# Performance work log

Measured on AMD Instinct MI355X. Metric: run time of the kernel, lower is better.

The kernel has to match this reference:

```python
import jax, jax.numpy as jnp
import numpy as np

N = 100000   # nodes
E = 3200000  # edges (before self-loops)
F = 128      # input feature dim
H = 2        # heads
C = 16       # hidden per head
G = 64       # graphs in batch
NEG_SLOPE = 0.2


def _gat_layer(x, src, dst, eattr, W, a_src, a_dst, W_e, a_e, bias):
    # x: [N, Fin]; W: [Fin, H*C]; eattr: [Et, 1]; W_e: [1, H*C]; a_*: [H, C]
    n = x.shape[0]
    h = (x @ W).reshape(n, H, C)                      # [N,H,C]
    asrc = jnp.sum(h * a_src, axis=-1)                # [N,H]
    adst = jnp.sum(h * a_dst, axis=-1)                # [N,H]
    he = (eattr @ W_e).reshape(-1, H, C)              # [Et,H,C]
    aedge = jnp.sum(he * a_e, axis=-1)                # [Et,H]
    alpha = jax.nn.leaky_relu(asrc[src] + adst[dst] + aedge, NEG_SLOPE)
    # segment softmax over incoming edges of each destination node
    m = jax.ops.segment_max(alpha, dst, num_segments=n)
    ex = jnp.exp(alpha - m[dst])
    s = jax.ops.segment_sum(ex, dst, num_segments=n)
    att = ex / (s[dst] + 1e-16)                        # [Et,H]
    msg = h[src] * att[:, :, None]                     # [Et,H,C]
    out = jax.ops.segment_sum(msg, dst, num_segments=n)  # [N,H,C]
    return out.reshape(n, H * C) + bias


def setup_inputs() -> dict:
    key = jax.random.key(0)
    ks = jax.random.split(key, 24)
    d = {
        'x': jax.random.normal(ks[0], (N, F), dtype=jnp.float32),
        'edge_index': jax.random.randint(ks[1], (2, E), 0, N, dtype=jnp.int64),
        'edge_attr': jax.random.normal(ks[2], (E, 1), dtype=jnp.float32),
        'batch': jnp.sort(jax.random.randint(ks[3], (N,), 0, G, dtype=jnp.int64)),
        # conv1: F -> H*C
        'W1': jax.random.normal(ks[4], (F, H * C), dtype=jnp.float32) * 0.1,
        'att_src1': jax.random.normal(ks[5], (H, C), dtype=jnp.float32) * 0.1,
        'att_dst1': jax.random.normal(ks[6], (H, C), dtype=jnp.float32) * 0.1,
        'We1': jax.random.normal(ks[7], (1, H * C), dtype=jnp.float32) * 0.1,
        'att_edge1': jax.random.normal(ks[8], (H, C), dtype=jnp.float32) * 0.1,
        'b1': jnp.zeros((H * C,), dtype=jnp.float32),
        # conv2: H*C -> H*C
        'W2': jax.random.normal(ks[9], (H * C, H * C), dtype=jnp.float32) * 0.1,
        'att_src2': jax.random.normal(ks[10], (H, C), dtype=jnp.float32) * 0.1,
        'att_dst2': jax.random.normal(ks[11], (H, C), dtype=jnp.float32) * 0.1,
        'We2': jax.random.normal(ks[12], (1, H * C), dtype=jnp.float32) * 0.1,
        'att_edge2': jax.random.normal(ks[13], (H, C), dtype=jnp.float32) * 0.1,
        'b2': jnp.zeros((H * C,), dtype=jnp.float32),
        # predictor MLP: 32 -> 32 -> 2
        'Wf1': jax.random.normal(ks[14], (H * C, 32), dtype=jnp.float32) * 0.1,
        'bf1': jnp.zeros((32,), dtype=jnp.float32),
        'Wf2': jax.random.normal(ks[15], (32, 2), dtype=jnp.float32) * 0.1,
        'bf2': jnp.zeros((2,), dtype=jnp.float32),
    }
    return d


def reference(x, edge_index, edge_attr, batch,
              W1, att_src1, att_dst1, We1, att_edge1, b1,
              W2, att_src2, att_dst2, We2, att_edge2, b2,
              Wf1, bf1, Wf2, bf2):
    n = x.shape[0]
    # PyG GATConv default: add self-loops with edge_attr fill_value='mean'
    loops = jnp.arange(n, dtype=edge_index.dtype)
    src = jnp.concatenate([edge_index[0], loops])
    dst = jnp.concatenate([edge_index[1], loops])
    ea = jnp.concatenate([edge_attr,
                          jnp.broadcast_to(edge_attr.mean(axis=0, keepdims=True), (n, 1))])
    h = _gat_layer(x, src, dst, ea, W1, att_src1, att_dst1, We1, att_edge1, b1)
    h = jax.nn.relu(h)  # dropout is identity in eval mode
    h = _gat_layer(h, src, dst, ea, W2, att_src2, att_dst2, We2, att_edge2, b2)
    # global mean pool over graphs
    sums = jax.ops.segment_sum(h, batch, num_segments=G)          # [G, H*C]
    cnt = jax.ops.segment_sum(jnp.ones((n,), h.dtype), batch, num_segments=G)
    emb = sums / jnp.maximum(cnt, 1.0)[:, None]
    # predictor MLP
    return jax.nn.relu(emb @ Wf1 + bf1) @ Wf2 + bf2               # [G, 2]
```

## Files before the change

kernel.cpp:

```cpp
#include <hip/hip_runtime.h>
#include <hip/hip_fp16.h>

#define N_NODES 100000
#define N_EDGES 3200000
#define F_IN    128
#define HC      32
#define CH      16
#define NGRAPH  64
#define NEG     0.2f

#define BSH   8
#define BNODE (1 << BSH)
#define NB2   ((N_NODES + BNODE - 1) >> BSH)
#define CAP   9216
#define EPB2  8192
#define BTHR  1024
#define HEPB  4096
#define GPAD  16
#define CHK   4096
#define NPB   512
#define GSPAN 16

__device__ __forceinline__ float lrelu(float x) { return x > 0.f ? x : NEG * x; }


__global__ void k_init(int* __restrict__ gcur, float* __restrict__ params,
                       float* __restrict__ gsums) {
    int t = threadIdx.x;
    if (t < NB2) gcur[t * GPAD] = t * CAP;
    if (t < 16) params[t] = 0.f;
    gsums[t] = 0.f;
    gsums[t + 1024] = 0.f;
}


__global__ __launch_bounds__(1024)
void k_bucket(const int* __restrict__ src, const int* __restrict__ dst,
              const float* __restrict__ ea, int* __restrict__ gcur,
              int2* __restrict__ staged, float* __restrict__ params) {
    __shared__ int lcur[NB2];
    __shared__ int lscan[512];
    __shared__ int gbase[NB2];
    __shared__ short rbkt[HEPB];
    __shared__ int2 recs[HEPB];
    int t = threadIdx.x;
    float acc = 0.f;
    for (int half = 0; half < 2; ++half) {
        int base = blockIdx.x * EPB2 + half * HEPB;
        for (int i = t; i < NB2; i += BTHR) lcur[i] = 0;
        __syncthreads();
        int  myb[HEPB / BTHR];
        int  myrank[HEPB / BTHR];
        int2 myrec[HEPB / BTHR];
#pragma unroll
        for (int i = 0; i < HEPB / BTHR; ++i) {
            int e = base + i * BTHR + t;
            myb[i] = -1;
            if (e < N_EDGES) {
                int dv = dst[e];
                float eav = ea[e];
                acc += eav;
                myb[i] = dv >> BSH;
                myrank[i] = atomicAdd(&lcur[myb[i]], 1);
                myrec[i] = make_int2((src[e] << BSH) | (dv & (BNODE - 1)),
                                     __float_as_int(eav));
            }
        }
        __syncthreads();
        if (t < 512) lscan[t] = (t < NB2) ? lcur[t] : 0;
        __syncthreads();
        for (int off = 1; off < 512; off <<= 1) {
            int u = 0;
            if (t < 512 && t >= off) u = lscan[t - off];
            __syncthreads();
            if (t < 512) lscan[t] += u;
            __syncthreads();
        }
        if (t < NB2 && lcur[t] > 0) gbase[t] = atomicAdd(&gcur[t * GPAD], lcur[t]);
        __syncthreads();
#pragma unroll
        for (int i = 0; i < HEPB / BTHR; ++i) {
            if (myb[i] >= 0) {
                int p = lscan[myb[i]] - lcur[myb[i]] + myrank[i];
                recs[p] = myrec[i];
                rbkt[p] = (short)myb[i];
            }
        }
        __syncthreads();
        int tot = lscan[511];
        for (int p = t; p < tot; p += BTHR) {
            int b = rbkt[p];
            int ex = lscan[b] - lcur[b];
            staged[gbase[b] + (p - ex)] = recs[p];
        }
        __syncthreads();
    }
    for (int m = 32; m >= 1; m >>= 1) acc += __shfl_xor(acc, m, 64);
    __shared__ float sh[BTHR / 64];
    int lane = t & 63, wid = t >> 6;
    if (lane == 0) sh[wid] = acc;
    __syncthreads();
    if (t == 0) {
        float s = 0.f;
        for (int i = 0; i < BTHR / 64; ++i) s += sh[i];
        unsafeAtomicAdd(&params[0], s);
    }
}


__global__ void k_setup(const float* __restrict__ We1, const float* __restrict__ ae1,
                        const float* __restrict__ We2, const float* __restrict__ ae2,
                        float* __restrict__ params, const int* __restrict__ gcur,
                        int* __restrict__ gstart, int* __restrict__ rowptr) {
    int t = threadIdx.x;
    if (t < 2) {
        float c1 = 0.f, c2 = 0.f;
        for (int c = 0; c < CH; ++c) {
            c1 += We1[t * CH + c] * ae1[t * CH + c];
            c2 += We2[t * CH + c] * ae2[t * CH + c];
        }
        params[2 + t] = c1;
        params[4 + t] = c2;
        if (t == 0) params[1] = params[0] / (float)N_EDGES;
    }
    __shared__ int sh[256];
    int v[2];
    int s = 0;
    for (int j = 0; j < 2; ++j) {
        int i = t * 2 + j;
        v[j] = (i < NB2) ? (gcur[i * GPAD] - i * CAP) : 0;
        s += v[j];
    }
    sh[t] = s;
    __syncthreads();
    for (int off = 1; off < 256; off <<= 1) {
        int u = (t >= off) ? sh[t - off] : 0;
        __syncthreads();
        sh[t] += u;
        __syncthreads();
    }
    int ex = sh[t] - s;
    for (int j = 0; j < 2; ++j) {
        int i = t * 2 + j;
        if (i < NB2) { gstart[i] = ex; ex += v[j]; }
    }
    if (t == 255) {
        gstart[NB2] = N_EDGES;
        rowptr[N_NODES] = N_EDGES;
    }
}


__global__ __launch_bounds__(1024)
void k_scatter(const int2* __restrict__ staged, const int* __restrict__ gcur,
               const int* __restrict__ gstart,
               int* __restrict__ rowptr, int2* __restrict__ epack) {
    __shared__ int cntl[BNODE];
    __shared__ int scanb[BNODE];
    __shared__ int cur[BNODE];
    __shared__ int cchist[BNODE];
    __shared__ int cexcl[BNODE];
    __shared__ short rbkt[CHK];
    __shared__ int2 recs[CHK];
    int b = blockIdx.x, t = threadIdx.x;
    int nbase = b << BSH;
    int bcount = N_NODES - nbase;
    if (bcount > BNODE) bcount = BNODE;
    int sbase = b * CAP;
    int en = gcur[b * GPAD];
    int st_true = gstart[b];
    if (t < BNODE) cntl[t] = 0;
    __syncthreads();
    for (int e = sbase + t; e < en; e += 1024)
        atomicAdd(&cntl[staged[e].x & (BNODE - 1)], 1);
    __syncthreads();
    if (t < BNODE) scanb[t] = cntl[t];
    __syncthreads();
    for (int off = 1; off < BNODE; off <<= 1) {
        int u = (t < BNODE && t >= off) ? scanb[t - off] : 0;
        __syncthreads();
        if (t < BNODE) scanb[t] += u;
        __syncthreads();
    }
    if (t < BNODE) {
        int ex = st_true + scanb[t] - cntl[t];
        cur[t] = ex;
        if (t < bcount) rowptr[nbase + t] = ex;
    }
    __syncthreads();
    int count = en - sbase;
    for (int cb = 0; cb < count; cb += CHK) {
        int clen = count - cb;
        if (clen > CHK) clen = CHK;
        if (t < BNODE) cchist[t] = 0;
        __syncthreads();
        int  mylo[CHK / 1024];
        int  myrank[CHK / 1024];
        int2 myrec[CHK / 1024];
#pragma unroll
        for (int i = 0; i < CHK / 1024; ++i) {
            int p = i * 1024 + t;
            mylo[i] = -1;
            if (p < clen) {
                int2 r = staged[sbase + cb + p];
                mylo[i] = r.x & (BNODE - 1);
                myrank[i] = atomicAdd(&cchist[mylo[i]], 1);
                myrec[i] = r;
            }
        }
        __syncthreads();
        if (t < BNODE) cexcl[t] = cchist[t];
        __syncthreads();
        for (int off = 1; off < BNODE; off <<= 1) {
            int u = (t < BNODE && t >= off) ? cexcl[t - off] : 0;
            __syncthreads();
            if (t < BNODE) cexcl[t] += u;
            __syncthreads();
        }
        if (t < BNODE) cexcl[t] -= cchist[t];
        __syncthreads();
#pragma unroll
        for (int i = 0; i < CHK / 1024; ++i) {
            if (mylo[i] >= 0) {
                int p = cexcl[mylo[i]] + myrank[i];
                recs[p] = myrec[i];
                rbkt[p] = (short)mylo[i];
            }
        }
        __syncthreads();
        for (int p = t; p < clen; p += 1024) {
            int lo = rbkt[p];
            epack[cur[lo] + (p - cexcl[lo])] = recs[p];
        }
        __syncthreads();
        if (t < BNODE) cur[t] += cchist[t];
        __syncthreads();
    }
}


#define COLS(ac, xv)                                                     \
    ac[0] = fmaf(xv.x, w0.x, ac[0]); ac[1] = fmaf(xv.x, w0.y, ac[1]);    \
    ac[2] = fmaf(xv.x, w0.z, ac[2]); ac[3] = fmaf(xv.x, w0.w, ac[3]);    \
    ac[0] = fmaf(xv.y, w1.x, ac[0]); ac[1] = fmaf(xv.y, w1.y, ac[1]);    \
    ac[2] = fmaf(xv.y, w1.z, ac[2]); ac[3] = fmaf(xv.y, w1.w, ac[3]);    \
    ac[0] = fmaf(xv.z, w2.x, ac[0]); ac[1] = fmaf(xv.z, w2.y, ac[1]);    \
    ac[2] = fmaf(xv.z, w2.z, ac[2]); ac[3] = fmaf(xv.z, w2.w, ac[3]);    \
    ac[0] = fmaf(xv.w, w3.x, ac[0]); ac[1] = fmaf(xv.w, w3.y, ac[1]);    \
    ac[2] = fmaf(xv.w, w3.z, ac[2]); ac[3] = fmaf(xv.w, w3.w, ac[3]);

template <int FIN>
__global__ __launch_bounds__(256)
void k_linear(const float* __restrict__ x, const float* __restrict__ W,
              const float* __restrict__ a_src, const float* __restrict__ a_dst,
              __half* __restrict__ h16, float* __restrict__ asrc,
              float* __restrict__ adst) {
    constexpr int PAD = FIN + 4;
    __shared__ float ws[FIN * HC];
    __shared__ float xs[64 * PAD];
    int t = threadIdx.x;
    int nbase = blockIdx.x * 64;
    int bcount = N_NODES - nbase;
    if (bcount > 64) bcount = 64;

    for (int i = t; i < FIN * HC / 4; i += 256)
        ((float4*)ws)[i] = ((const float4*)W)[i];
    const float4* xg = (const float4*)(x + (size_t)nbase * FIN);
    int nf4 = bcount * FIN / 4;
    for (int i = t; i < 64 * FIN / 4; i += 256) {
        if (i < nf4) {
            float4 v = xg[i];
            int flat = i * 4;
            int row = flat / FIN, col = flat % FIN;
            *(float4*)&xs[row * PAD + col] = v;
        }
    }
    __syncthreads();

    int cg = t & 7, np = t >> 3;
    int n0 = np * 2, n1 = n0 + 1;
    float acc0[4] = {0.f, 0.f, 0.f, 0.f};
    float acc1[4] = {0.f, 0.f, 0.f, 0.f};
#pragma unroll
    for (int k = 0; k < FIN; k += 4) {
        float4 xa = *(const float4*)&xs[n0 * PAD + k];
        float4 xb = *(const float4*)&xs[n1 * PAD + k];
        const float4* wp = (const float4*)&ws[k * HC] + cg;
        float4 w0 = wp[0], w1 = wp[8], w2 = wp[16], w3 = wp[24];
        COLS(acc0, xa)
        COLS(acc1, xb)
    }

    int hh = cg >> 2;
    float s0 = 0.f, d0 = 0.f, s1 = 0.f, d1 = 0.f;
#pragma unroll
    for (int j = 0; j < 4; ++j) {
        float av = a_src[hh * CH + (cg & 3) * 4 + j];
        float dv = a_dst[hh * CH + (cg & 3) * 4 + j];
        s0 = fmaf(acc0[j], av, s0); d0 = fmaf(acc0[j], dv, d0);
        s1 = fmaf(acc1[j], av, s1); d1 = fmaf(acc1[j], dv, d1);
    }
    s0 += __shfl_xor(s0, 1, 64); s0 += __shfl_xor(s0, 2, 64);
    d0 += __shfl_xor(d0, 1, 64); d0 += __shfl_xor(d0, 2, 64);
    s1 += __shfl_xor(s1, 1, 64); s1 += __shfl_xor(s1, 2, 64);
    d1 += __shfl_xor(d1, 1, 64); d1 += __shfl_xor(d1, 2, 64);

    if (n0 < bcount) {
        __half2 pa = __floats2half2_rn(acc0[0], acc0[1]);
        __half2 pb = __floats2half2_rn(acc0[2], acc0[3]);
        *(uint2*)&h16[(size_t)(nbase + n0) * HC + cg * 4] =
            make_uint2(*(unsigned*)&pa, *(unsigned*)&pb);
        if ((cg & 3) == 0) {
            asrc[(nbase + n0) * 2 + hh] = s0;
            adst[(nbase + n0) * 2 + hh] = d0;
        }
    }
    if (n1 < bcount) {
        __half2 pa = __floats2half2_rn(acc1[0], acc1[1]);
        __half2 pb = __floats2half2_rn(acc1[2], acc1[3]);
        *(uint2*)&h16[(size_t)(nbase + n1) * HC + cg * 4] =
            make_uint2(*(unsigned*)&pa, *(unsigned*)&pb);
        if ((cg & 3) == 0) {
            asrc[(nbase + n1) * 2 + hh] = s1;
            adst[(nbase + n1) * 2 + hh] = d1;
        }
    }
}


#define FMA4(ACC, WGT, VEC)                                                      \
    ACC.x = fmaf(WGT, VEC.x, ACC.x); ACC.y = fmaf(WGT, VEC.y, ACC.y);            \
    ACC.z = fmaf(WGT, VEC.z, ACC.z); ACC.w = fmaf(WGT, VEC.w, ACC.w);

__device__ __forceinline__ void unpack8(uint4 hv, float4& p, float4& u) {
    float2 f0 = __half22float2(*(__half2*)&hv.x);
    float2 f1 = __half22float2(*(__half2*)&hv.y);
    float2 f2 = __half22float2(*(__half2*)&hv.z);
    float2 f3 = __half22float2(*(__half2*)&hv.w);
    p = make_float4(f0.x, f0.y, f1.x, f1.y);
    u = make_float4(f2.x, f2.y, f3.x, f3.y);
}

template <int FUSE>
__global__ __launch_bounds__(256)
void k_gat(const int* __restrict__ rowptr, const int2* __restrict__ epack,
           const __half* __restrict__ h16,
           const float* __restrict__ asrc, const float* __restrict__ adst,
           const float* __restrict__ params, int ceoff,
           const float* __restrict__ bias, int do_relu,
           float* __restrict__ outf, __half* __restrict__ outh,
           const float* __restrict__ W2,
           const float* __restrict__ as2, const float* __restrict__ ad2,
           float* __restrict__ asrc2, float* __restrict__ adst2) {
    __shared__ float w2s[FUSE ? HC * HC : 4];
    int t = threadIdx.x;
    if (FUSE) {
        for (int i = t; i < HC * HC / 4; i += 256)
            ((float4*)w2s)[i] = ((const float4*)W2)[i];
        __syncthreads();
    }
    int tid = blockIdx.x * blockDim.x + t;
    int n = tid >> 4;
    if (n >= N_NODES) return;
    int q = tid & 15;
    int chan = q & 3, quarter = q >> 2, hh = chan >> 1;
    int st = rowptr[n], en = rowptr[n + 1];
    int len = en - st;
    int q0 = st + ((len * quarter) >> 2);
    int q1 = st + ((len * (quarter + 1)) >> 2);
    float ce = params[ceoff + hh];
    float adn = adst[n * 2 + hh];
    const uint4* h4v = (const uint4*)h16;
    float4 A0 = make_float4(0.f, 0.f, 0.f, 0.f);
    float4 A1 = make_float4(0.f, 0.f, 0.f, 0.f);
    float ssum = 0.f;
    for (int e = q0; e < q1; e += 4) {
        int e1 = e + 1, e2 = e + 2, e3 = e + 3;
        int i1 = e1 < q1 ? e1 : q1 - 1;
        int i2 = e2 < q1 ? e2 : q1 - 1;
        int i3 = e3 < q1 ? e3 : q1 - 1;
        int2 r0 = epack[e], r1 = epack[i1], r2 = epack[i2], r3 = epack[i3];
        int s0 = r0.x >> BSH, s1 = r1.x >> BSH, s2 = r2.x >> BSH, s3 = r3.x >> BSH;
        float a0 = asrc[s0 * 2 + hh], a1 = asrc[s1 * 2 + hh];
        float a2 = asrc[s2 * 2 + hh], a3 = asrc[s3 * 2 + hh];
        uint4 hv0 = h4v[s0 * 4 + chan];
        uint4 hv1 = h4v[s1 * 4 + chan];
        uint4 hv2 = h4v[s2 * 4 + chan];
        uint4 hv3 = h4v[s3 * 4 + chan];
        float g0 = __expf(lrelu(a0 + adn + ce * __int_as_float(r0.y)));
        float g1 = __expf(lrelu(a1 + adn + ce * __int_as_float(r1.y)));
        float g2 = __expf(lrelu(a2 + adn + ce * __int_as_float(r2.y)));
        float g3 = __expf(lrelu(a3 + adn + ce * __int_as_float(r3.y)));
        g1 = (e1 < q1) ? g1 : 0.f;
        g2 = (e2 < q1) ? g2 : 0.f;
        g3 = (e3 < q1) ? g3 : 0.f;
        float4 p0, u0, p1, u1, p2, u2, p3, u3;
        unpack8(hv0, p0, u0); unpack8(hv1, p1, u1);
        unpack8(hv2, p2, u2); unpack8(hv3, p3, u3);
        FMA4(A0, g0, p0) FMA4(A1, g0, u0) ssum += g0;
        FMA4(A0, g1, p1) FMA4(A1, g1, u1) ssum += g1;
        FMA4(A0, g2, p2) FMA4(A1, g2, u2) ssum += g2;
        FMA4(A0, g3, p3) FMA4(A1, g3, u3) ssum += g3;
    }
    if (quarter == 0) {
        float gself = __expf(lrelu(asrc[n * 2 + hh] + adn + ce * params[1]));
        float4 psf, usf;
        unpack8(h4v[n * 4 + chan], psf, usf);
        FMA4(A0, gself, psf) FMA4(A1, gself, usf)
        ssum += gself;
    }
    A0.x += __shfl_xor(A0.x, 4, 64); A0.y += __shfl_xor(A0.y, 4, 64);
    A0.z += __shfl_xor(A0.z, 4, 64); A0.w += __shfl_xor(A0.w, 4, 64);
    A1.x += __shfl_xor(A1.x, 4, 64); A1.y += __shfl_xor(A1.y, 4, 64);
    A1.z += __shfl_xor(A1.z, 4, 64); A1.w += __shfl_xor(A1.w, 4, 64);
    ssum += __shfl_xor(ssum, 4, 64);
    A0.x += __shfl_xor(A0.x, 8, 64); A0.y += __shfl_xor(A0.y, 8, 64);
    A0.z += __shfl_xor(A0.z, 8, 64); A0.w += __shfl_xor(A0.w, 8, 64);
    A1.x += __shfl_xor(A1.x, 8, 64); A1.y += __shfl_xor(A1.y, 8, 64);
    A1.z += __shfl_xor(A1.z, 8, 64); A1.w += __shfl_xor(A1.w, 8, 64);
    ssum += __shfl_xor(ssum, 8, 64);
    if (quarter != 0) return;
    float inv = 1.f / (ssum + 1e-16f);
    int b4 = chan * 2;
    float4 bv0 = ((const float4*)bias)[b4], bv1 = ((const float4*)bias)[b4 + 1];
    float4 v0 = make_float4(A0.x * inv + bv0.x, A0.y * inv + bv0.y,
                            A0.z * inv + bv0.z, A0.w * inv + bv0.w);
    float4 v1 = make_float4(A1.x * inv + bv1.x, A1.y * inv + bv1.y,
                            A1.z * inv + bv1.z, A1.w * inv + bv1.w);
    if (do_relu) {
        v0.x = fmaxf(v0.x, 0.f); v0.y = fmaxf(v0.y, 0.f);
        v0.z = fmaxf(v0.z, 0.f); v0.w = fmaxf(v0.w, 0.f);
        v1.x = fmaxf(v1.x, 0.f); v1.y = fmaxf(v1.y, 0.f);
        v1.z = fmaxf(v1.z, 0.f); v1.w = fmaxf(v1.w, 0.f);
    }
    if (!FUSE) {
        ((float4*)outf)[n * 8 + b4] = v0;
        ((float4*)outf)[n * 8 + b4 + 1] = v1;
        return;
    }
    int lane = t & 63;
    int bse = lane & 48;
    float h2[8] = {0.f, 0.f, 0.f, 0.f, 0.f, 0.f, 0.f, 0.f};
#pragma unroll
    for (int cc = 0; cc < 4; ++cc) {
        int sl = bse | cc;
        float vv[8];
        vv[0] = __shfl(v0.x, sl, 64); vv[1] = __shfl(v0.y, sl, 64);
        vv[2] = __shfl(v0.z, sl, 64); vv[3] = __shfl(v0.w, sl, 64);
        vv[4] = __shfl(v1.x, sl, 64); vv[5] = __shfl(v1.y, sl, 64);
        vv[6] = __shfl(v1.z, sl, 64); vv[7] = __shfl(v1.w, sl, 64);
#pragma unroll
        for (int m = 0; m < 8; ++m) {
            const float* wrow = &w2s[(cc * 8 + m) * HC + chan * 8];
            float4 wa = *(const float4*)&wrow[0];
            float4 wb = *(const float4*)&wrow[4];
            h2[0] = fmaf(vv[m], wa.x, h2[0]); h2[1] = fmaf(vv[m], wa.y, h2[1]);
            h2[2] = fmaf(vv[m], wa.z, h2[2]); h2[3] = fmaf(vv[m], wa.w, h2[3]);
            h2[4] = fmaf(vv[m], wb.x, h2[4]); h2[5] = fmaf(vv[m], wb.y, h2[5]);
            h2[6] = fmaf(vv[m], wb.z, h2[6]); h2[7] = fmaf(vv[m], wb.w, h2[7]);
        }
    }
    __half2 q0h = __floats2half2_rn(h2[0], h2[1]);
    __half2 q1h = __floats2half2_rn(h2[2], h2[3]);
    __half2 q2h = __floats2half2_rn(h2[4], h2[5]);
    __half2 q3h = __floats2half2_rn(h2[6], h2[7]);
    *(uint4*)&outh[(size_t)n * HC + chan * 8] =
        make_uint4(*(unsigned*)&q0h, *(unsigned*)&q1h,
                   *(unsigned*)&q2h, *(unsigned*)&q3h);
    float s2 = 0.f, d2 = 0.f;
#pragma unroll
    for (int j = 0; j < 8; ++j) {
        s2 = fmaf(h2[j], as2[chan * 8 + j], s2);
        d2 = fmaf(h2[j], ad2[chan * 8 + j], d2);
    }
    s2 += __shfl_xor(s2, 1, 64);
    d2 += __shfl_xor(d2, 1, 64);
    if ((chan & 1) == 0) {
        asrc2[n * 2 + (chan >> 1)] = s2;
        adst2[n * 2 + (chan >> 1)] = d2;
    }
}


__global__ __launch_bounds__(1024)
void k_pool1(const float* __restrict__ feat, const int* __restrict__ batch,
             float* __restrict__ gsums) {
    __shared__ float gsum[GSPAN][32];
    int t = threadIdx.x;
    int c = t & 31, r = t >> 5;
    int base = blockIdx.x * NPB;
    if (t < GSPAN * 32) ((float*)gsum)[t] = 0.f;
    __syncthreads();
    int g0 = batch[base];
    float acc = 0.f;
    int gprev = -1;
    for (int i = 0; i < NPB / 32; ++i) {
        int n = base + r * (NPB / 32) + i;
        if (n >= N_NODES) break;
        int g = batch[n] - g0;
        if (g != gprev) {
            if (gprev >= 0) {
                if (gprev < GSPAN) atomicAdd(&gsum[gprev][c], acc);
                else unsafeAtomicAdd(&gsums[(g0 + gprev) * 32 + c], acc);
            }
            acc = 0.f;
            gprev = g;
        }
        acc += feat[(size_t)n * HC + c];
    }
    if (gprev >= 0) {
        if (gprev < GSPAN) atomicAdd(&gsum[gprev][c], acc);
        else unsafeAtomicAdd(&gsums[(g0 + gprev) * 32 + c], acc);
    }
    __syncthreads();
    if (t < GSPAN * 32) {
        int gi = t >> 5, cc = t & 31;
        float v = gsum[gi][cc];
        if (v != 0.f && g0 + gi < NGRAPH)
            unsafeAtomicAdd(&gsums[(g0 + gi) * 32 + cc], v);
    }
}


__global__ void k_mlp(const float* __restrict__ gsums, const int* __restrict__ batch,
                      const float* __restrict__ Wf1, const float* __restrict__ bf1,
                      const float* __restrict__ Wf2, const float* __restrict__ bf2,
                      float* __restrict__ out) {
    int g = blockIdx.x;
    __shared__ int sse[2];
    __shared__ float emb[32];
    __shared__ float hid[32];
    if (threadIdx.x < 2) {
        int target = g + (int)threadIdx.x;
        int lo = 0, hi = N_NODES;
        while (lo < hi) {
            int mid = (lo + hi) >> 1;
            if (batch[mid] < target) lo = mid + 1; else hi = mid;
        }
        sse[threadIdx.x] = lo;
    }
    __syncthreads();
    int cnt = sse[1] - sse[0];
    if (threadIdx.x < 32)
        emb[threadIdx.x] = gsums[g * 32 + threadIdx.x] / (float)(cnt > 0 ? cnt : 1);
    __syncthreads();
    if (threadIdx.x < 32) {
        int j = threadIdx.x;
        float a = bf1[j];
        for (int k = 0; k < 32; ++k) a = fmaf(emb[k], Wf1[k * 32 + j], a);
        hid[j] = fmaxf(a, 0.f);
    }
    __syncthreads();
    if (threadIdx.x < 2) {
        int j = threadIdx.x;
        float o = bf2[j];
        for (int k = 0; k < 32; ++k) o = fmaf(hid[k], Wf2[k * 2 + j], o);
        out[g * 2 + j] = o;
    }
}

extern "C" void kernel_launch(void* const* d_in, const int* in_sizes, int n_in,
                              void* d_out, int out_size, void* d_ws, size_t ws_size,
                              hipStream_t stream) {
    const float* x   = (const float*)d_in[0];
    const int*   ei  = (const int*)d_in[1];
    const float* ea  = (const float*)d_in[2];
    const int* batch = (const int*)d_in[3];
    const float* W1  = (const float*)d_in[4];
    const float* as1 = (const float*)d_in[5];
    const float* ad1 = (const float*)d_in[6];
    const float* We1 = (const float*)d_in[7];
    const float* ae1 = (const float*)d_in[8];
    const float* b1  = (const float*)d_in[9];
    const float* W2  = (const float*)d_in[10];
    const float* as2 = (const float*)d_in[11];
    const float* ad2 = (const float*)d_in[12];
    const float* We2 = (const float*)d_in[13];
    const float* ae2 = (const float*)d_in[14];
    const float* b2  = (const float*)d_in[15];
    const float* Wf1 = (const float*)d_in[16];
    const float* bf1 = (const float*)d_in[17];
    const float* Wf2 = (const float*)d_in[18];
    const float* bf2 = (const float*)d_in[19];
    float* out = (float*)d_out;
    (void)in_sizes; (void)n_in; (void)out_size; (void)ws_size;

    const int* srcp = ei;
    const int* dstp = ei + N_EDGES;

    char* wsb = (char*)d_ws;
    size_t off = 0;
    auto alloc = [&](size_t bytes) -> char* {
        char* p = wsb + off;
        off = (off + bytes + 255) & ~(size_t)255;
        return p;
    };
    float* params = (float*)alloc(64);
    char* regA = alloc((size_t)NB2 * CAP * 8 + 4096);
    int2*  staged = (int2*)regA;
    float* feat   = (float*)regA;
    int2*  epack  = (int2*)alloc((size_t)N_EDGES * 8);
    __half* h16a  = (__half*)alloc((size_t)N_NODES * HC * 2);
    __half* h16b  = (__half*)alloc((size_t)N_NODES * HC * 2);
    float* asrc   = (float*)alloc((size_t)N_NODES * 2 * 4);
    float* adst   = (float*)alloc((size_t)N_NODES * 2 * 4);
    float* asrc2  = (float*)alloc((size_t)N_NODES * 2 * 4);
    float* adst2  = (float*)alloc((size_t)N_NODES * 2 * 4);
    int*   gstart = (int*)alloc((size_t)(NB2 + 1) * 4);
    int*   gcur   = (int*)alloc((size_t)NB2 * GPAD * 4);
    int*   rowptr = (int*)alloc((size_t)(N_NODES + 1) * 4);
    float* gsums  = (float*)alloc((size_t)NGRAPH * HC * 4);

    const int nBlkB = (N_EDGES + EPB2 - 1) / EPB2;
    const int nBlkL = (N_NODES + 63) / 64;
    const int nBlkG = (N_NODES * 16 + 255) / 256;
    const int nBlkP = (N_NODES + NPB - 1) / NPB;

    k_init<<<1, 1024, 0, stream>>>(gcur, params, gsums);
    k_bucket<<<nBlkB, BTHR, 0, stream>>>(srcp, dstp, ea, gcur, staged, params);
    k_setup<<<1, 256, 0, stream>>>(We1, ae1, We2, ae2, params, gcur, gstart, rowptr);
    k_scatter<<<NB2, 1024, 0, stream>>>(staged, gcur, gstart, rowptr, epack);

    k_linear<F_IN><<<nBlkL, 256, 0, stream>>>(x, W1, as1, ad1, h16a, asrc, adst);
    k_gat<1><<<nBlkG, 256, 0, stream>>>(rowptr, epack, h16a, asrc, adst, params, 2, b1, 1,
                                        nullptr, h16b, W2, as2, ad2, asrc2, adst2);

    k_gat<0><<<nBlkG, 256, 0, stream>>>(rowptr, epack, h16b, asrc2, adst2, params, 4, b2, 0,
                                        feat, nullptr, W2, as2, ad2, asrc2, adst2);

    k_pool1<<<nBlkP, 1024, 0, stream>>>(feat, batch, gsums);
    k_mlp<<<NGRAPH, 64, 0, stream>>>(gsums, batch, Wf1, bf1, Wf2, bf2, out);
}
```

Before: 338.3 us.

## Split edge records into index and fp16 attr arrays, use wave-shuffle scans

The packed int2 edge array is split into a 32-bit index array and an fp16 edge-attribute array. This cuts the bytes the two GAT kernels read per edge from 8 to 6. The block-wide shared-memory Hillis-Steele scans in bucketing and scatter are replaced by wavefront shuffle scans plus a small cross-wave fixup, which removes many barriers. The bucket kernel also processes one 4096-edge half per block instead of looping over two, doubling the block count and the global atomics on bucket cursors. Storing edge attributes in fp16 loses some precision in the attention logits.

```diff
diff --git a/kernel.cpp b/kernel.cpp
--- a/kernel.cpp
+++ b/kernel.cpp
@@ -13,15 +13,23 @@
 #define BNODE (1 << BSH)
 #define NB2   ((N_NODES + BNODE - 1) >> BSH)
 #define CAP   9216
-#define EPB2  8192
+#define EPB   4096
 #define BTHR  1024
-#define HEPB  4096
 #define GPAD  16
 #define CHK   4096
 #define NPB   512
 #define GSPAN 16
 
 __device__ __forceinline__ float lrelu(float x) { return x > 0.f ? x : NEG * x; }
+
+__device__ __forceinline__ int wscan(int v) {
+#pragma unroll
+    for (int off = 1; off < 64; off <<= 1) {
+        int u = __shfl_up(v, off, 64);
+        if ((int)(threadIdx.x & 63) >= off) v += u;
+    }
+    return v;
+}
 
 
 __global__ void k_init(int* __restrict__ gcur, float* __restrict__ params,
@@ -41,59 +49,58 @@
     __shared__ int lcur[NB2];
     __shared__ int lscan[512];
     __shared__ int gbase[NB2];
-    __shared__ short rbkt[HEPB];
-    __shared__ int2 recs[HEPB];
+    __shared__ int wsum[8];
+    __shared__ short rbkt[EPB];
+    __shared__ int2 recs[EPB];
     int t = threadIdx.x;
+    int base = blockIdx.x * EPB;
     float acc = 0.f;
-    for (int half = 0; half < 2; ++half) {
-        int base = blockIdx.x * EPB2 + half * HEPB;
-        for (int i = t; i < NB2; i += BTHR) lcur[i] = 0;
-        __syncthreads();
-        int  myb[HEPB / BTHR];
-        int  myrank[HEPB / BTHR];
-        int2 myrec[HEPB / BTHR];
-#pragma unroll
-        for (int i = 0; i < HEPB / BTHR; ++i) {
-            int e = base + i * BTHR + t;
-            myb[i] = -1;
-            if (e < N_EDGES) {
-                int dv = dst[e];
-                float eav = ea[e];
-                acc += eav;
-                myb[i] = dv >> BSH;
-                myrank[i] = atomicAdd(&lcur[myb[i]], 1);
-                myrec[i] = make_int2((src[e] << BSH) | (dv & (BNODE - 1)),
-                                     __float_as_int(eav));
-            }
-        }
-        __syncthreads();
-        if (t < 512) lscan[t] = (t < NB2) ? lcur[t] : 0;
-        __syncthreads();
-        for (int off = 1; off < 512; off <<= 1) {
-            int u = 0;
-            if (t < 512 && t >= off) u = lscan[t - off];
-            __syncthreads();
-            if (t < 512) lscan[t] += u;
-            __syncthreads();
-        }
-        if (t < NB2 && lcur[t] > 0) gbase[t] = atomicAdd(&gcur[t * GPAD], lcur[t]);
-        __syncthreads();
-#pragma unroll
-        for (int i = 0; i < HEPB / BTHR; ++i) {
-            if (myb[i] >= 0) {
-                int p = lscan[myb[i]] - lcur[myb[i]] + myrank[i];
-                recs[p] = myrec[i];
-                rbkt[p] = (short)myb[i];
-            }
-        }
-        __syncthreads();
-        int tot = lscan[511];
-        for (int p = t; p < tot; p += BTHR) {
-            int b = rbkt[p];
-            int ex = lscan[b] - lcur[b];
-            staged[gbase[b] + (p - ex)] = recs[p];
-        }
-        __syncthreads();
+    for (int i = t; i < NB2; i += BTHR) lcur[i] = 0;
+    __syncthreads();
+    int  myb[EPB / BTHR];
+    int  myrank[EPB / BTHR];
+    int2 myrec[EPB / BTHR];
+#pragma unroll
+    for (int i = 0; i < EPB / BTHR; ++i) {
+        int e = base + i * BTHR + t;
+        myb[i] = -1;
+        if (e < N_EDGES) {
+            int dv = dst[e];
+            float eav = ea[e];
+            acc += eav;
+            myb[i] = dv >> BSH;
+            myrank[i] = atomicAdd(&lcur[myb[i]], 1);
+            myrec[i] = make_int2((src[e] << BSH) | (dv & (BNODE - 1)),
+                                 __float_as_int(eav));
+        }
+    }
+    __syncthreads();
+    int v = 0;
+    if (t < 512) v = (t < NB2) ? lcur[t] : 0;
+    int sv = wscan(v);
+    if (t < 512 && (t & 63) == 63) wsum[t >> 6] = sv;
+    if (t < NB2 && lcur[t] > 0) gbase[t] = atomicAdd(&gcur[t * GPAD], lcur[t]);
+    __syncthreads();
+    if (t < 512) {
+        int bb = 0;
+        for (int i = 0; i < (t >> 6); ++i) bb += wsum[i];
+        lscan[t] = sv + bb;
+    }
+    __syncthreads();
+#pragma unroll
+    for (int i = 0; i < EPB / BTHR; ++i) {
+        if (myb[i] >= 0) {
+            int p = lscan[myb[i]] - lcur[myb[i]] + myrank[i];
+            recs[p] = myrec[i];
+            rbkt[p] = (short)myb[i];
+        }
+    }
+    __syncthreads();
+    int tot = lscan[511];
+    for (int p = t; p < tot; p += BTHR) {
+        int b = rbkt[p];
+        int ex = lscan[b] - lcur[b];
+        staged[gbase[b] + (p - ex)] = recs[p];
     }
     for (int m = 32; m >= 1; m >>= 1) acc += __shfl_xor(acc, m, 64);
     __shared__ float sh[BTHR / 64];
@@ -154,12 +161,13 @@
 __global__ __launch_bounds__(1024)
 void k_scatter(const int2* __restrict__ staged, const int* __restrict__ gcur,
                const int* __restrict__ gstart,
-               int* __restrict__ rowptr, int2* __restrict__ epack) {
+               int* __restrict__ rowptr, int* __restrict__ eidx,
+               __half* __restrict__ eea) {
     __shared__ int cntl[BNODE];
-    __shared__ int scanb[BNODE];
     __shared__ int cur[BNODE];
     __shared__ int cchist[BNODE];
     __shared__ int cexcl[BNODE];
+    __shared__ int ws4[4];
     __shared__ short rbkt[CHK];
     __shared__ int2 recs[CHK];
     int b = blockIdx.x, t = threadIdx.x;
@@ -174,20 +182,20 @@
     for (int e = sbase + t; e < en; e += 1024)
         atomicAdd(&cntl[staged[e].x & (BNODE - 1)], 1);
     __syncthreads();
-    if (t < BNODE) scanb[t] = cntl[t];
-    __syncthreads();
-    for (int off = 1; off < BNODE; off <<= 1) {
-        int u = (t < BNODE && t >= off) ? scanb[t - off] : 0;
-        __syncthreads();
-        if (t < BNODE) scanb[t] += u;
-        __syncthreads();
-    }
-    if (t < BNODE) {
-        int ex = st_true + scanb[t] - cntl[t];
-        cur[t] = ex;
-        if (t < bcount) rowptr[nbase + t] = ex;
-    }
-    __syncthreads();
+    {
+        int v = (t < BNODE) ? cntl[t] : 0;
+        int sv = wscan(v);
+        if (t < BNODE && (t & 63) == 63) ws4[t >> 6] = sv;
+        __syncthreads();
+        if (t < BNODE) {
+            int bb = 0;
+            for (int i = 0; i < (t >> 6); ++i) bb += ws4[i];
+            int ex = st_true + sv + bb - v;
+            cur[t] = ex;
+            if (t < bcount) rowptr[nbase + t] = ex;
+        }
+        __syncthreads();
+    }
     int count = en - sbase;
     for (int cb = 0; cb < count; cb += CHK) {
         int clen = count - cb;
@@ -209,16 +217,18 @@
             }
         }
         __syncthreads();
-        if (t < BNODE) cexcl[t] = cchist[t];
-        __syncthreads();
-        for (int off = 1; off < BNODE; off <<= 1) {
-            int u = (t < BNODE && t >= off) ? cexcl[t - off] : 0;
+        {
+            int v = (t < BNODE) ? cchist[t] : 0;
+            int sv = wscan(v);
+            if (t < BNODE && (t & 63) == 63) ws4[t >> 6] = sv;
             __syncthreads();
-            if (t < BNODE) cexcl[t] += u;
+            if (t < BNODE) {
+                int bb = 0;
+                for (int i = 0; i < (t >> 6); ++i) bb += ws4[i];
+                cexcl[t] = sv + bb - v;
+            }
             __syncthreads();
         }
-        if (t < BNODE) cexcl[t] -= cchist[t];
-        __syncthreads();
 #pragma unroll
         for (int i = 0; i < CHK / 1024; ++i) {
             if (mylo[i] >= 0) {
@@ -230,7 +240,10 @@
         __syncthreads();
         for (int p = t; p < clen; p += 1024) {
             int lo = rbkt[p];
-            epack[cur[lo] + (p - cexcl[lo])] = recs[p];
+            int pos = cur[lo] + (p - cexcl[lo]);
+            int2 r = recs[p];
+            eidx[pos] = r.x;
+            eea[pos] = __float2half(__int_as_float(r.y));
         }
         __syncthreads();
         if (t < BNODE) cur[t] += cchist[t];
@@ -343,8 +356,8 @@
 
 template <int FUSE>
 __global__ __launch_bounds__(256)
-void k_gat(const int* __restrict__ rowptr, const int2* __restrict__ epack,
-           const __half* __restrict__ h16,
+void k_gat(const int* __restrict__ rowptr, const int* __restrict__ eidx,
+           const __half* __restrict__ eea, const __half* __restrict__ h16,
            const float* __restrict__ asrc, const float* __restrict__ adst,
            const float* __restrict__ params, int ceoff,
            const float* __restrict__ bias, int do_relu,
@@ -379,18 +392,20 @@
         int i1 = e1 < q1 ? e1 : q1 - 1;
         int i2 = e2 < q1 ? e2 : q1 - 1;
         int i3 = e3 < q1 ? e3 : q1 - 1;
-        int2 r0 = epack[e], r1 = epack[i1], r2 = epack[i2], r3 = epack[i3];
-        int s0 = r0.x >> BSH, s1 = r1.x >> BSH, s2 = r2.x >> BSH, s3 = r3.x >> BSH;
+        int r0 = eidx[e], r1 = eidx[i1], r2 = eidx[i2], r3 = eidx[i3];
+        float ea0 = __half2float(eea[e]),  ea1 = __half2float(eea[i1]);
+        float ea2 = __half2float(eea[i2]), ea3 = __half2float(eea[i3]);
+        int s0 = r0 >> BSH, s1 = r1 >> BSH, s2 = r2 >> BSH, s3 = r3 >> BSH;
         float a0 = asrc[s0 * 2 + hh], a1 = asrc[s1 * 2 + hh];
         float a2 = asrc[s2 * 2 + hh], a3 = asrc[s3 * 2 + hh];
         uint4 hv0 = h4v[s0 * 4 + chan];
         uint4 hv1 = h4v[s1 * 4 + chan];
         uint4 hv2 = h4v[s2 * 4 + chan];
         uint4 hv3 = h4v[s3 * 4 + chan];
-        float g0 = __expf(lrelu(a0 + adn + ce * __int_as_float(r0.y)));
-        float g1 = __expf(lrelu(a1 + adn + ce * __int_as_float(r1.y)));
-        float g2 = __expf(lrelu(a2 + adn + ce * __int_as_float(r2.y)));
-        float g3 = __expf(lrelu(a3 + adn + ce * __int_as_float(r3.y)));
+        float g0 = __expf(lrelu(a0 + adn + ce * ea0));
+        float g1 = __expf(lrelu(a1 + adn + ce * ea1));
+        float g2 = __expf(lrelu(a2 + adn + ce * ea2));
+        float g3 = __expf(lrelu(a3 + adn + ce * ea3));
         g1 = (e1 < q1) ? g1 : 0.f;
         g2 = (e2 < q1) ? g2 : 0.f;
         g3 = (e3 < q1) ? g3 : 0.f;
@@ -599,7 +614,8 @@
     char* regA = alloc((size_t)NB2 * CAP * 8 + 4096);
     int2*  staged = (int2*)regA;
     float* feat   = (float*)regA;
-    int2*  epack  = (int2*)alloc((size_t)N_EDGES * 8);
+    int*   eidx   = (int*)alloc((size_t)N_EDGES * 4);
+    __half* eea   = (__half*)alloc((size_t)N_EDGES * 2);
     __half* h16a  = (__half*)alloc((size_t)N_NODES * HC * 2);
     __half* h16b  = (__half*)alloc((size_t)N_NODES * HC * 2);
     float* asrc   = (float*)alloc((size_t)N_NODES * 2 * 4);
@@ -611,7 +627,7 @@
     int*   rowptr = (int*)alloc((size_t)(N_NODES + 1) * 4);
     float* gsums  = (float*)alloc((size_t)NGRAPH * HC * 4);
 
-    const int nBlkB = (N_EDGES + EPB2 - 1) / EPB2;
+    const int nBlkB = (N_EDGES + EPB - 1) / EPB;
     const int nBlkL = (N_NODES + 63) / 64;
     const int nBlkG = (N_NODES * 16 + 255) / 256;
     const int nBlkP = (N_NODES + NPB - 1) / NPB;
@@ -619,13 +635,13 @@
     k_init<<<1, 1024, 0, stream>>>(gcur, params, gsums);
     k_bucket<<<nBlkB, BTHR, 0, stream>>>(srcp, dstp, ea, gcur, staged, params);
     k_setup<<<1, 256, 0, stream>>>(We1, ae1, We2, ae2, params, gcur, gstart, rowptr);
-    k_scatter<<<NB2, 1024, 0, stream>>>(staged, gcur, gstart, rowptr, epack);
+    k_scatter<<<NB2, 1024, 0, stream>>>(staged, gcur, gstart, rowptr, eidx, eea);
 
     k_linear<F_IN><<<nBlkL, 256, 0, stream>>>(x, W1, as1, ad1, h16a, asrc, adst);
-    k_gat<1><<<nBlkG, 256, 0, stream>>>(rowptr, epack, h16a, asrc, adst, params, 2, b1, 1,
+    k_gat<1><<<nBlkG, 256, 0, stream>>>(rowptr, eidx, eea, h16a, asrc, adst, params, 2, b1, 1,
                                         nullptr, h16b, W2, as2, ad2, asrc2, adst2);
 
-    k_gat<0><<<nBlkG, 256, 0, stream>>>(rowptr, epack, h16b, asrc2, adst2, params, 4, b2, 0,
+    k_gat<0><<<nBlkG, 256, 0, stream>>>(rowptr, eidx, eea, h16b, asrc2, adst2, params, 4, b2, 0,
                                         feat, nullptr, W2, as2, ad2, asrc2, adst2);
 
     k_pool1<<<nBlkP, 1024, 0, stream>>>(feat, batch, gsums);
```

Result: no change. 334.0 us (-1.3%).
